# Kernel optimization log

Measured on AMD Instinct MI355X. Metric: run time of the kernel, lower is better.

The kernel has to match this reference:

```python
import jax, jax.numpy as jnp
import numpy as np

DIM = 1024
HID = 2732  # int(2*4*1024/3) rounded up to multiple of 4
E = 8
TOPK = 2
B, S = 2, 2048


def setup_inputs() -> dict:
    key = jax.random.key(0)
    ks = jax.random.split(key, 5)
    scale = 0.02
    return {
        "x": jax.random.normal(ks[0], (B, S, DIM), dtype=jnp.float32),
        "Wg": jax.random.normal(ks[1], (E, DIM), dtype=jnp.float32) * scale,
        "W1": jax.random.normal(ks[2], (E, HID, DIM), dtype=jnp.float32) * scale,
        "W2": jax.random.normal(ks[3], (E, DIM, HID), dtype=jnp.float32) * scale,
        "W3": jax.random.normal(ks[4], (E, HID, DIM), dtype=jnp.float32) * scale,
    }


def reference(x, Wg, W1, W2, W3):
    b, s, d = x.shape
    xt = x.reshape(b * s, d)                              # [N, d]
    scores = xt @ Wg.T                                    # [N, E]
    w, idx = jax.lax.top_k(scores, TOPK)                  # [N, k]
    w = jax.nn.softmax(w, axis=-1)
    n = xt.shape[0]
    # combine weights scattered back into [N, E] (top-k indices are distinct per row)
    cw = jnp.zeros((n, E), dtype=x.dtype).at[jnp.arange(n)[:, None], idx].set(w)
    # dense per-expert SwiGLU (mathematically identical to masked dispatch)
    h1 = jnp.einsum('nd,ehd->neh', xt, W1)                # [N, E, H]
    h3 = jnp.einsum('nd,ehd->neh', xt, W3)
    h = jax.nn.silu(h1) * h3
    y = jnp.einsum('neh,edh->ned', h, W2)                 # [N, E, d]
    out = jnp.einsum('ned,ne->nd', y, cw)                 # [N, d]
    return out
```

## Files before the change

kernel.cpp:

```cpp
#include <hip/hip_runtime.h>
#include <hip/hip_bf16.h>
#include <stdint.h>

#define DIM   1024
#define HID   2732
#define HPAD  2752
#define NEXP  8
#define NTOK  4096
#define NROW  8192

#define G13   (NEXP * HPAD * (DIM / 4))
#define GALL  (2 * G13)
#define G2    (NEXP * DIM * (HPAD / 4))
#define CONV13_BLKS 2048
#define CONV2_BLKS  1024
#define ROUTE_BLKS  (NTOK / 4)

typedef __attribute__((ext_vector_type(8))) short bf16x8;
typedef __attribute__((ext_vector_type(4))) float f32x4;

__device__ __forceinline__ unsigned short f2bf(float f) {
    union { float f; uint32_t u; } v; v.f = f;
    uint32_t u = v.u;
    return (unsigned short)((u + 0x7FFFu + ((u >> 16) & 1u)) >> 16);
}
__device__ __forceinline__ float bf2f(unsigned short h) {
    union { uint32_t u; float f; } v; v.u = ((uint32_t)h) << 16;
    return v.f;
}

#define ASYNC_CP16(g, l) __builtin_amdgcn_global_load_lds( \
    (const __attribute__((address_space(1))) void*)(g), \
    (__attribute__((address_space(3))) void*)(l), 16, 0, 0)

__global__ void prep1_kernel(const float* __restrict__ x,  const float* __restrict__ Wg,
                             const float* __restrict__ W1, const float* __restrict__ W3,
                             unsigned short* __restrict__ W1b,
                             unsigned short* __restrict__ W3b,
                             int* __restrict__ counts, int* __restrict__ a_exp,
                             int* __restrict__ a_rank, float* __restrict__ a_w) {
    int b = blockIdx.x;
    if (b < CONV13_BLKS) {
        const uint32_t nthr = CONV13_BLKS * 256;
        uint32_t t0 = (uint32_t)b * 256 + threadIdx.x;
        for (uint32_t g0 = t0; g0 < (uint32_t)GALL; g0 += nthr * 4) {
            float4 v[4]; uint32_t gs[4]; bool ok[4];
#pragma unroll
            for (int k = 0; k < 4; ++k) {
                uint32_t g = g0 + (uint32_t)k * nthr;
                gs[k] = g; ok[k] = g < (uint32_t)GALL;
                v[k] = (float4){0.f, 0.f, 0.f, 0.f};
                if (ok[k]) {
                    uint32_t gg = g < (uint32_t)G13 ? g : g - (uint32_t)G13;
                    const float* src = g < (uint32_t)G13 ? W1 : W3;
                    uint32_t d4 = gg & 255;
                    uint32_t rest = gg >> 8;
                    uint32_t hp = rest % HPAD;
                    uint32_t e  = rest / HPAD;
                    if (hp < HID)
                        v[k] = *(const float4*)(src + ((size_t)e * HID + hp) * DIM + d4 * 4);
                }
            }
#pragma unroll
            for (int k = 0; k < 4; ++k) {
                if (ok[k]) {
                    unsigned short* dst = gs[k] < (uint32_t)G13 ? W1b : W3b;
                    uint32_t gg = gs[k] < (uint32_t)G13 ? gs[k] : gs[k] - (uint32_t)G13;
                    ushort4 o;
                    o.x = f2bf(v[k].x); o.y = f2bf(v[k].y);
                    o.z = f2bf(v[k].z); o.w = f2bf(v[k].w);
                    *(ushort4*)(dst + (size_t)gg * 4) = o;
                }
            }
        }
        return;
    }
    b -= CONV13_BLKS;
    int wave = threadIdx.x >> 6, lane = threadIdx.x & 63;
    int n = b * 4 + wave;
    const float* xr = x + (size_t)n * DIM + lane * 16;
    float p[NEXP];
#pragma unroll
    for (int e = 0; e < NEXP; ++e) p[e] = 0.f;
#pragma unroll
    for (int i = 0; i < 4; ++i) {
        float4 xv = *(const float4*)(xr + i * 4);
#pragma unroll
        for (int e = 0; e < NEXP; ++e) {
            float4 wv = *(const float4*)(Wg + e * DIM + lane * 16 + i * 4);
            p[e] += xv.x * wv.x + xv.y * wv.y + xv.z * wv.z + xv.w * wv.w;
        }
    }
#pragma unroll
    for (int off = 32; off > 0; off >>= 1)
#pragma unroll
        for (int e = 0; e < NEXP; ++e) p[e] += __shfl_xor(p[e], off);
    if (lane == 0) {
        int i1 = -1, i2 = -1; float m1 = -1e30f, m2 = -1e30f;
#pragma unroll
        for (int e = 0; e < NEXP; ++e) {
            float s = p[e];
            if (s > m1) { m2 = m1; i2 = i1; m1 = s; i1 = e; }
            else if (s > m2) { m2 = s; i2 = e; }
        }
        float e2 = __expf(m2 - m1);
        float inv = 1.f / (1.f + e2);
        int a = n * 2;
        a_exp[a] = i1;  a_w[a] = inv;        a_rank[a] = atomicAdd(&counts[i1], 1);
        a_exp[a+1] = i2; a_w[a+1] = e2 * inv; a_rank[a+1] = atomicAdd(&counts[i2], 1);
    }
}

__global__ void conv2_kernel(const float* __restrict__ W2,
                             unsigned short* __restrict__ W2b) {
    const uint32_t nthr = CONV2_BLKS * 256;
    uint32_t t0 = (uint32_t)blockIdx.x * 256 + threadIdx.x;
    for (uint32_t g0 = t0; g0 < (uint32_t)G2; g0 += nthr * 4) {
        float4 v[4]; uint32_t gs[4]; bool ok[4];
#pragma unroll
        for (int k = 0; k < 4; ++k) {
            uint32_t g = g0 + (uint32_t)k * nthr;
            gs[k] = g; ok[k] = g < (uint32_t)G2;
            v[k] = (float4){0.f, 0.f, 0.f, 0.f};
            if (ok[k]) {
                uint32_t h4 = g % (HPAD / 4);
                uint32_t rest = g / (HPAD / 4);
                uint32_t d = rest & (DIM - 1);
                uint32_t e = rest >> 10;
                if (h4 * 4 < HID)
                    v[k] = *(const float4*)(W2 + ((size_t)e * DIM + d) * HID + h4 * 4);
            }
        }
#pragma unroll
        for (int k = 0; k < 4; ++k) {
            if (ok[k]) {
                ushort4 o;
                o.x = f2bf(v[k].x); o.y = f2bf(v[k].y);
                o.z = f2bf(v[k].z); o.w = f2bf(v[k].w);
                *(ushort4*)(W2b + (size_t)gs[k] * 4) = o;
            }
        }
    }
}

__global__ void gather_kernel(const float* __restrict__ x, const int* __restrict__ a_exp,
                              const int* __restrict__ a_rank,
                              const int* __restrict__ counts,
                              unsigned short* __restrict__ XG,
                              int* __restrict__ row_of_a) {
    __shared__ int soff[NEXP];
    if (threadIdx.x == 0) {
        int s = 0;
#pragma unroll
        for (int e = 0; e < NEXP; ++e) { soff[e] = s; s += counts[e]; }
    }
    __syncthreads();
    int a = blockIdx.x, n = a >> 1;
    int row = soff[a_exp[a]] + a_rank[a];
    if (threadIdx.x == 0) row_of_a[a] = row;
    float4 xv = *(const float4*)(x + (size_t)n * DIM + threadIdx.x * 4);
    ushort4 o; o.x = f2bf(xv.x); o.y = f2bf(xv.y); o.z = f2bf(xv.z); o.w = f2bf(xv.w);
    *(ushort4*)(XG + (size_t)row * DIM + threadIdx.x * 4) = o;
}

__global__ __launch_bounds__(256, 2) void gemm1_kernel(
    const unsigned short* __restrict__ XG,
    const unsigned short* __restrict__ W1b,
    const unsigned short* __restrict__ W3b,
    const int* __restrict__ counts,
    unsigned short* __restrict__ Hbuf)
{
    const int e = blockIdx.z, mtile = blockIdx.y, ntile = blockIdx.x;
    const int cnt = counts[e];
    if (mtile * 128 >= cnt) return;
    int rowstart = 0;
    for (int i = 0; i < e; ++i) rowstart += counts[i];
    rowstart += mtile * 128;

    __shared__ __align__(16) unsigned short As[128 * 64];
    __shared__ __align__(16) unsigned short B1s[64 * 64];
    __shared__ __align__(16) unsigned short B3s[64 * 64];

    const int tid = threadIdx.x, lane = tid & 63, wave = tid >> 6;
    const int wm = wave >> 1, wn = wave & 1;
    const int quad = lane >> 4;

    const unsigned short* w1e = W1b + (size_t)e * HPAD * DIM;
    const unsigned short* w3e = W3b + (size_t)e * HPAD * DIM;

    const int srow = tid >> 3;
    const int scol = (((tid & 7) ^ (srow & 7)) * 8);
    const unsigned short* ag[4];
#pragma unroll
    for (int r = 0; r < 4; ++r) {
        int grow = rowstart + r * 32 + srow;
        if (grow > NROW - 1) grow = NROW - 1;
        ag[r] = XG + (size_t)grow * DIM + scol;
    }
    const unsigned short* bg1[2]; const unsigned short* bg3[2];
#pragma unroll
    for (int r = 0; r < 2; ++r) {
        int grow = ntile * 64 + r * 32 + srow;
        bg1[r] = w1e + (size_t)grow * DIM + scol;
        bg3[r] = w3e + (size_t)grow * DIM + scol;
    }

    f32x4 acc1[4][2], acc3[4][2];
#pragma unroll
    for (int i = 0; i < 4; ++i)
#pragma unroll
        for (int j = 0; j < 2; ++j) {
            acc1[i][j] = (f32x4){0.f, 0.f, 0.f, 0.f};
            acc3[i][j] = (f32x4){0.f, 0.f, 0.f, 0.f};
        }

    for (int kk = 0; kk < DIM / 64; ++kk) {
        const int k0 = kk * 64;
#pragma unroll
        for (int r = 0; r < 4; ++r)
            ASYNC_CP16(ag[r] + k0, &As[r * 2048 + tid * 8]);
#pragma unroll
        for (int r = 0; r < 2; ++r) {
            ASYNC_CP16(bg1[r] + k0, &B1s[r * 2048 + tid * 8]);
            ASYNC_CP16(bg3[r] + k0, &B3s[r * 2048 + tid * 8]);
        }
        __syncthreads();
#pragma unroll
        for (int ks = 0; ks < 2; ++ks) {
            const int cbase = ks * 4 + quad;
            bf16x8 af[4], b1f[2], b3f[2];
#pragma unroll
            for (int i = 0; i < 4; ++i) {
                int rl = wm * 64 + i * 16 + (lane & 15);
                af[i] = *(const bf16x8*)&As[rl * 64 + ((cbase ^ (rl & 7)) * 8)];
            }
#pragma unroll
            for (int j = 0; j < 2; ++j) {
                int rl1 = wn * 32 + j * 16 + (lane & 15);
                b1f[j] = *(const bf16x8*)&B1s[rl1 * 64 + ((cbase ^ (rl1 & 7)) * 8)];
                b3f[j] = *(const bf16x8*)&B3s[rl1 * 64 + ((cbase ^ (rl1 & 7)) * 8)];
            }
#pragma unroll
            for (int i = 0; i < 4; ++i)
#pragma unroll
                for (int j = 0; j < 2; ++j) {
                    acc1[i][j] = __builtin_amdgcn_mfma_f32_16x16x32_bf16(af[i], b1f[j], acc1[i][j], 0, 0, 0);
                    acc3[i][j] = __builtin_amdgcn_mfma_f32_16x16x32_bf16(af[i], b3f[j], acc3[i][j], 0, 0, 0);
                }
        }
        __syncthreads();
    }

    int mvalid = cnt - mtile * 128; if (mvalid > 128) mvalid = 128;
#pragma unroll
    for (int i = 0; i < 4; ++i)
#pragma unroll
        for (int r = 0; r < 4; ++r) {
            int rl = wm * 64 + i * 16 + quad * 4 + r;
            if (rl < mvalid) {
                size_t rowg = (size_t)(rowstart + rl);
#pragma unroll
                for (int j = 0; j < 2; ++j) {
                    float v1 = acc1[i][j][r], v3 = acc3[i][j][r];
                    float s = v1 / (1.f + __expf(-v1));
                    Hbuf[rowg * HPAD + ntile * 64 + wn * 32 + j * 16 + (lane & 15)] = f2bf(s * v3);
                }
            }
        }
}

__global__ __launch_bounds__(256, 2) void gemm2_kernel(
    const unsigned short* __restrict__ Hbuf,
    const unsigned short* __restrict__ W2b,
    const int* __restrict__ counts,
    unsigned short* __restrict__ Ybuf)
{
    const int e = blockIdx.z, mtile = blockIdx.y, ntile = blockIdx.x;
    const int cnt = counts[e];
    if (mtile * 128 >= cnt) return;
    int rowstart = 0;
    for (int i = 0; i < e; ++i) rowstart += counts[i];
    rowstart += mtile * 128;

    __shared__ __align__(16) unsigned short As[128 * 64];
    __shared__ __align__(16) unsigned short Bs[128 * 64];

    const int tid = threadIdx.x, lane = tid & 63, wave = tid >> 6;
    const int wm = wave >> 1, wn = wave & 1;
    const int quad = lane >> 4;

    const unsigned short* w2e = W2b + (size_t)e * DIM * HPAD;
    const int srow = tid >> 3;
    const int scol = (((tid & 7) ^ (srow & 7)) * 8);
    const unsigned short* ag[4]; const unsigned short* bg[4];
#pragma unroll
    for (int r = 0; r < 4; ++r) {
        int grow = rowstart + r * 32 + srow;
        if (grow > NROW - 1) grow = NROW - 1;
        ag[r] = Hbuf + (size_t)grow * HPAD + scol;
        bg[r] = w2e + (size_t)(ntile * 128 + r * 32 + srow) * HPAD + scol;
    }

    f32x4 acc[4][4];
#pragma unroll
    for (int i = 0; i < 4; ++i)
#pragma unroll
        for (int j = 0; j < 4; ++j) acc[i][j] = (f32x4){0.f, 0.f, 0.f, 0.f};

    for (int kk = 0; kk < HPAD / 64; ++kk) {
        const int k0 = kk * 64;
#pragma unroll
        for (int r = 0; r < 4; ++r) {
            ASYNC_CP16(ag[r] + k0, &As[r * 2048 + tid * 8]);
            ASYNC_CP16(bg[r] + k0, &Bs[r * 2048 + tid * 8]);
        }
        __syncthreads();
#pragma unroll
        for (int ks = 0; ks < 2; ++ks) {
            const int cbase = ks * 4 + quad;
            bf16x8 af[4], bf[4];
#pragma unroll
            for (int i = 0; i < 4; ++i) {
                int rla = wm * 64 + i * 16 + (lane & 15);
                int rlb = wn * 64 + i * 16 + (lane & 15);
                af[i] = *(const bf16x8*)&As[rla * 64 + ((cbase ^ (rla & 7)) * 8)];
                bf[i] = *(const bf16x8*)&Bs[rlb * 64 + ((cbase ^ (rlb & 7)) * 8)];
            }
#pragma unroll
            for (int i = 0; i < 4; ++i)
#pragma unroll
                for (int j = 0; j < 4; ++j)
                    acc[i][j] = __builtin_amdgcn_mfma_f32_16x16x32_bf16(af[i], bf[j], acc[i][j], 0, 0, 0);
        }
        __syncthreads();
    }

    int mvalid = cnt - mtile * 128; if (mvalid > 128) mvalid = 128;
#pragma unroll
    for (int i = 0; i < 4; ++i)
#pragma unroll
        for (int r = 0; r < 4; ++r) {
            int rl = wm * 64 + i * 16 + quad * 4 + r;
            if (rl < mvalid) {
                int rowg = rowstart + rl;
                unsigned short* yrow = Ybuf + (size_t)rowg * DIM + ntile * 128 + wn * 64 + (lane & 15);
#pragma unroll
                for (int j = 0; j < 4; ++j)
                    yrow[j * 16] = f2bf(acc[i][j][r]);
            }
        }
}

__global__ void combine_kernel(const unsigned short* __restrict__ Ybuf,
                               const int* __restrict__ row_of_a,
                               const float* __restrict__ a_w,
                               float* __restrict__ out) {
    int n = blockIdx.x, t = threadIdx.x;
    int r0 = row_of_a[2 * n], r1 = row_of_a[2 * n + 1];
    float w0 = a_w[2 * n], w1 = a_w[2 * n + 1];
    ushort4 y0 = *(const ushort4*)(Ybuf + (size_t)r0 * DIM + t * 4);
    ushort4 y1 = *(const ushort4*)(Ybuf + (size_t)r1 * DIM + t * 4);
    float4 o;
    o.x = w0 * bf2f(y0.x) + w1 * bf2f(y1.x);
    o.y = w0 * bf2f(y0.y) + w1 * bf2f(y1.y);
    o.z = w0 * bf2f(y0.z) + w1 * bf2f(y1.z);
    o.w = w0 * bf2f(y0.w) + w1 * bf2f(y1.w);
    *(float4*)(out + (size_t)n * DIM + t * 4) = o;
}

extern "C" void kernel_launch(void* const* d_in, const int* in_sizes, int n_in,
                              void* d_out, int out_size, void* d_ws, size_t ws_size,
                              hipStream_t stream) {
    const float* x  = (const float*)d_in[0];
    const float* Wg = (const float*)d_in[1];
    const float* W1 = (const float*)d_in[2];
    const float* W2 = (const float*)d_in[3];
    const float* W3 = (const float*)d_in[4];
    float* out = (float*)d_out;

    char* ws = (char*)d_ws;
    size_t off = 0;
    auto alloc = [&](size_t bytes) -> void* {
        void* p = ws + off;
        off = (off + bytes + 255) & ~(size_t)255;
        return p;
    };
    int*   counts      = (int*)alloc(NEXP * 4);
    int*   a_exp       = (int*)alloc(NROW * 4);
    int*   a_rank      = (int*)alloc(NROW * 4);
    float* a_w         = (float*)alloc(NROW * 4);
    int*   row_of_a    = (int*)alloc(NROW * 4);
    unsigned short* XG   = (unsigned short*)alloc((size_t)NROW * DIM * 2);
    unsigned short* Hbuf = (unsigned short*)alloc((size_t)NROW * HPAD * 2);
    unsigned short* W1b  = (unsigned short*)alloc((size_t)NEXP * HPAD * DIM * 2);
    unsigned short* W3b  = (unsigned short*)alloc((size_t)NEXP * HPAD * DIM * 2);
    unsigned short* W2b  = (unsigned short*)alloc((size_t)NEXP * DIM * HPAD * 2);
    unsigned short* Ybuf = (unsigned short*)W1b;

    hipMemsetAsync(counts, 0, NEXP * 4, stream);

    prep1_kernel<<<CONV13_BLKS + ROUTE_BLKS, 256, 0, stream>>>(
        x, Wg, W1, W3, W1b, W3b, counts, a_exp, a_rank, a_w);
    gather_kernel<<<NROW, 256, 0, stream>>>(x, a_exp, a_rank, counts, XG, row_of_a);

    gemm1_kernel<<<dim3(HPAD / 64, 64, NEXP), 256, 0, stream>>>(
        XG, W1b, W3b, counts, Hbuf);
    conv2_kernel<<<CONV2_BLKS, 256, 0, stream>>>(W2, W2b);
    gemm2_kernel<<<dim3(DIM / 128, 64, NEXP), 256, 0, stream>>>(
        Hbuf, W2b, counts, Ybuf);
    combine_kernel<<<NTOK, 256, 0, stream>>>(Ybuf, row_of_a, a_w, out);
}
```

Baseline: 622.4 us.

## Fold W2 conversion into gemm1 grid and reorder tile dispatch

The W2 fp32-to-bf16 conversion moves into an extra z-slice of the gemm1 launch, so it can overlap with gemm1 tiles instead of running as its own kernel. The W1/W3 conversion now iterates over the source layout with 8-wide loads and stores, and separate blocks zero the padding rows. The grid is reordered so the m-tile index is blockIdx.x with the m-tile count capped at 32, which removes many empty early-exit blocks and changes the order tiles are scheduled in. The risk is that conversion blocks compete with GEMM tiles for bandwidth and compute units.

```diff
diff --git a/kernel.cpp b/kernel.cpp
--- a/kernel.cpp
+++ b/kernel.cpp
@@ -9,12 +9,16 @@
 #define NTOK  4096
 #define NROW  8192
 
-#define G13   (NEXP * HPAD * (DIM / 4))
-#define GALL  (2 * G13)
+#define G8ONE (NEXP * HID * (DIM / 8))
+#define G8ALL (2 * G8ONE)
 #define G2    (NEXP * DIM * (HPAD / 4))
-#define CONV13_BLKS 2048
-#define CONV2_BLKS  1024
+#define PADG  (2 * NEXP * (HPAD - HID) * (DIM / 8))
+
+#define CONV13_BLKS 4096
+#define PAD_BLKS    64
 #define ROUTE_BLKS  (NTOK / 4)
+#define MT_MAX      32
+#define CONV2_CB    (MT_MAX * 43)
 
 typedef __attribute__((ext_vector_type(8))) short bf16x8;
 typedef __attribute__((ext_vector_type(4))) float f32x4;
@@ -43,39 +47,54 @@
     if (b < CONV13_BLKS) {
         const uint32_t nthr = CONV13_BLKS * 256;
         uint32_t t0 = (uint32_t)b * 256 + threadIdx.x;
-        for (uint32_t g0 = t0; g0 < (uint32_t)GALL; g0 += nthr * 4) {
-            float4 v[4]; uint32_t gs[4]; bool ok[4];
+        for (uint32_t g0 = t0; g0 < (uint32_t)G8ALL; g0 += nthr * 4) {
+            float4 va[4], vb[4]; uint32_t gs[4]; bool ok[4];
 #pragma unroll
             for (int k = 0; k < 4; ++k) {
                 uint32_t g = g0 + (uint32_t)k * nthr;
-                gs[k] = g; ok[k] = g < (uint32_t)GALL;
-                v[k] = (float4){0.f, 0.f, 0.f, 0.f};
+                gs[k] = g; ok[k] = g < (uint32_t)G8ALL;
                 if (ok[k]) {
-                    uint32_t gg = g < (uint32_t)G13 ? g : g - (uint32_t)G13;
-                    const float* src = g < (uint32_t)G13 ? W1 : W3;
-                    uint32_t d4 = gg & 255;
-                    uint32_t rest = gg >> 8;
-                    uint32_t hp = rest % HPAD;
-                    uint32_t e  = rest / HPAD;
-                    if (hp < HID)
-                        v[k] = *(const float4*)(src + ((size_t)e * HID + hp) * DIM + d4 * 4);
+                    uint32_t gg = g < (uint32_t)G8ONE ? g : g - (uint32_t)G8ONE;
+                    const float* src = g < (uint32_t)G8ONE ? W1 : W3;
+                    const float* p = src + (size_t)gg * 8;
+                    va[k] = *(const float4*)p;
+                    vb[k] = *(const float4*)(p + 4);
                 }
             }
 #pragma unroll
             for (int k = 0; k < 4; ++k) {
                 if (ok[k]) {
-                    unsigned short* dst = gs[k] < (uint32_t)G13 ? W1b : W3b;
-                    uint32_t gg = gs[k] < (uint32_t)G13 ? gs[k] : gs[k] - (uint32_t)G13;
-                    ushort4 o;
-                    o.x = f2bf(v[k].x); o.y = f2bf(v[k].y);
-                    o.z = f2bf(v[k].z); o.w = f2bf(v[k].w);
-                    *(ushort4*)(dst + (size_t)gg * 4) = o;
+                    uint32_t gg = gs[k] < (uint32_t)G8ONE ? gs[k] : gs[k] - (uint32_t)G8ONE;
+                    unsigned short* dst = gs[k] < (uint32_t)G8ONE ? W1b : W3b;
+                    uint32_t d8 = gg & 127, row = gg >> 7;
+                    uint32_t e = row / HID;
+                    size_t off = ((size_t)row + 20u * e) * DIM + d8 * 8;
+                    bf16x8 o;
+                    o[0] = (short)f2bf(va[k].x); o[1] = (short)f2bf(va[k].y);
+                    o[2] = (short)f2bf(va[k].z); o[3] = (short)f2bf(va[k].w);
+                    o[4] = (short)f2bf(vb[k].x); o[5] = (short)f2bf(vb[k].y);
+                    o[6] = (short)f2bf(vb[k].z); o[7] = (short)f2bf(vb[k].w);
+                    *(bf16x8*)(dst + off) = o;
                 }
             }
         }
         return;
     }
     b -= CONV13_BLKS;
+    if (b < PAD_BLKS) {
+        const uint32_t nthr = PAD_BLKS * 256;
+        bf16x8 z = {0, 0, 0, 0, 0, 0, 0, 0};
+        for (uint32_t g = (uint32_t)b * 256 + threadIdx.x; g < (uint32_t)PADG; g += nthr) {
+            uint32_t half = (uint32_t)PADG / 2;
+            unsigned short* dst = g < half ? W1b : W3b;
+            uint32_t gg = g < half ? g : g - half;
+            uint32_t d8 = gg & 127, prow = gg >> 7;
+            uint32_t e = prow / 20, h = HID + prow % 20;
+            *(bf16x8*)(dst + ((size_t)e * HPAD + h) * DIM + d8 * 8) = z;
+        }
+        return;
+    }
+    b -= PAD_BLKS;
     int wave = threadIdx.x >> 6, lane = threadIdx.x & 63;
     int n = b * 4 + wave;
     const float* xr = x + (size_t)n * DIM + lane * 16;
@@ -108,38 +127,6 @@
         int a = n * 2;
         a_exp[a] = i1;  a_w[a] = inv;        a_rank[a] = atomicAdd(&counts[i1], 1);
         a_exp[a+1] = i2; a_w[a+1] = e2 * inv; a_rank[a+1] = atomicAdd(&counts[i2], 1);
-    }
-}
-
-__global__ void conv2_kernel(const float* __restrict__ W2,
-                             unsigned short* __restrict__ W2b) {
-    const uint32_t nthr = CONV2_BLKS * 256;
-    uint32_t t0 = (uint32_t)blockIdx.x * 256 + threadIdx.x;
-    for (uint32_t g0 = t0; g0 < (uint32_t)G2; g0 += nthr * 4) {
-        float4 v[4]; uint32_t gs[4]; bool ok[4];
-#pragma unroll
-        for (int k = 0; k < 4; ++k) {
-            uint32_t g = g0 + (uint32_t)k * nthr;
-            gs[k] = g; ok[k] = g < (uint32_t)G2;
-            v[k] = (float4){0.f, 0.f, 0.f, 0.f};
-            if (ok[k]) {
-                uint32_t h4 = g % (HPAD / 4);
-                uint32_t rest = g / (HPAD / 4);
-                uint32_t d = rest & (DIM - 1);
-                uint32_t e = rest >> 10;
-                if (h4 * 4 < HID)
-                    v[k] = *(const float4*)(W2 + ((size_t)e * DIM + d) * HID + h4 * 4);
-            }
-        }
-#pragma unroll
-        for (int k = 0; k < 4; ++k) {
-            if (ok[k]) {
-                ushort4 o;
-                o.x = f2bf(v[k].x); o.y = f2bf(v[k].y);
-                o.z = f2bf(v[k].z); o.w = f2bf(v[k].w);
-                *(ushort4*)(W2b + (size_t)gs[k] * 4) = o;
-            }
-        }
     }
 }
 
@@ -163,14 +150,49 @@
     *(ushort4*)(XG + (size_t)row * DIM + threadIdx.x * 4) = o;
 }
 
-__global__ __launch_bounds__(256, 2) void gemm1_kernel(
+__global__ __launch_bounds__(256, 2) void gemm1_conv2_kernel(
     const unsigned short* __restrict__ XG,
     const unsigned short* __restrict__ W1b,
     const unsigned short* __restrict__ W3b,
+    const float* __restrict__ W2,
+    unsigned short* __restrict__ W2b,
     const int* __restrict__ counts,
     unsigned short* __restrict__ Hbuf)
 {
-    const int e = blockIdx.z, mtile = blockIdx.y, ntile = blockIdx.x;
+    if (blockIdx.z == NEXP) {
+        const uint32_t nthr = CONV2_CB * 256;
+        uint32_t lid = blockIdx.y * MT_MAX + blockIdx.x;
+        uint32_t t0 = lid * 256 + threadIdx.x;
+        for (uint32_t g0 = t0; g0 < (uint32_t)G2; g0 += nthr * 4) {
+            float4 v[4]; uint32_t gs[4]; bool ok[4];
+#pragma unroll
+            for (int k = 0; k < 4; ++k) {
+                uint32_t g = g0 + (uint32_t)k * nthr;
+                gs[k] = g; ok[k] = g < (uint32_t)G2;
+                v[k] = (float4){0.f, 0.f, 0.f, 0.f};
+                if (ok[k]) {
+                    uint32_t h4 = g % (HPAD / 4);
+                    uint32_t rest = g / (HPAD / 4);
+                    uint32_t d = rest & (DIM - 1);
+                    uint32_t e = rest >> 10;
+                    if (h4 * 4 < HID)
+                        v[k] = *(const float4*)(W2 + ((size_t)e * DIM + d) * HID + h4 * 4);
+                }
+            }
+#pragma unroll
+            for (int k = 0; k < 4; ++k) {
+                if (ok[k]) {
+                    ushort4 o;
+                    o.x = f2bf(v[k].x); o.y = f2bf(v[k].y);
+                    o.z = f2bf(v[k].z); o.w = f2bf(v[k].w);
+                    *(ushort4*)(W2b + (size_t)gs[k] * 4) = o;
+                }
+            }
+        }
+        return;
+    }
+
+    const int e = blockIdx.z, mtile = blockIdx.x, ntile = blockIdx.y;
     const int cnt = counts[e];
     if (mtile * 128 >= cnt) return;
     int rowstart = 0;
@@ -275,7 +297,7 @@
     const int* __restrict__ counts,
     unsigned short* __restrict__ Ybuf)
 {
-    const int e = blockIdx.z, mtile = blockIdx.y, ntile = blockIdx.x;
+    const int e = blockIdx.z, mtile = blockIdx.x, ntile = blockIdx.y;
     const int cnt = counts[e];
     if (mtile * 128 >= cnt) return;
     int rowstart = 0;
@@ -399,14 +421,13 @@
 
     hipMemsetAsync(counts, 0, NEXP * 4, stream);
 
-    prep1_kernel<<<CONV13_BLKS + ROUTE_BLKS, 256, 0, stream>>>(
+    prep1_kernel<<<CONV13_BLKS + PAD_BLKS + ROUTE_BLKS, 256, 0, stream>>>(
         x, Wg, W1, W3, W1b, W3b, counts, a_exp, a_rank, a_w);
     gather_kernel<<<NROW, 256, 0, stream>>>(x, a_exp, a_rank, counts, XG, row_of_a);
 
-    gemm1_kernel<<<dim3(HPAD / 64, 64, NEXP), 256, 0, stream>>>(
-        XG, W1b, W3b, counts, Hbuf);
-    conv2_kernel<<<CONV2_BLKS, 256, 0, stream>>>(W2, W2b);
-    gemm2_kernel<<<dim3(DIM / 128, 64, NEXP), 256, 0, stream>>>(
+    gemm1_conv2_kernel<<<dim3(MT_MAX, HPAD / 64, NEXP + 1), 256, 0, stream>>>(
+        XG, W1b, W3b, W2, W2b, counts, Hbuf);
+    gemm2_kernel<<<dim3(MT_MAX, DIM / 128, NEXP), 256, 0, stream>>>(
         Hbuf, W2b, counts, Ybuf);
     combine_kernel<<<NTOK, 256, 0, stream>>>(Ybuf, row_of_a, a_w, out);
 }
```

After: 823.8 us. 1.32x slower.
